# Performance work log

Measured on AMD Instinct MI355X. Metric: run time of the kernel, lower is better.

Reference implementation:

```python
import jax, jax.numpy as jnp
import numpy as np

N_NODES = 100000
N_EDGES = 1600000
IN_CH = 128
HID = 128
NUM_CLASSES = 10
NUM_GRAPHS = 128
SLOPE = 0.01  # F.leaky_relu default negative_slope


def _lin_params(key, fan_in, fan_out):
    kw, kb = jax.random.split(key)
    bound = 1.0 / np.sqrt(fan_in)
    W = jax.random.uniform(kw, (fan_in, fan_out), jnp.float32, -bound, bound)
    b = jax.random.uniform(kb, (fan_out,), jnp.float32, -bound, bound)
    return W, b


def setup_inputs() -> dict:
    key = jax.random.key(0)
    ks = jax.random.split(key, 8)
    x = jax.random.normal(ks[0], (N_NODES, IN_CH), jnp.float32)
    edge_index = jax.random.randint(ks[1], (2, N_EDGES), 0, N_NODES, jnp.int64)
    batch = jnp.sort(jax.random.randint(ks[2], (N_NODES,), 0, NUM_GRAPHS, jnp.int64))
    W1, b1 = _lin_params(ks[3], IN_CH, HID)
    W2, b2 = _lin_params(ks[4], HID, HID)
    W3, b3 = _lin_params(ks[5], HID, HID // 2)
    W4, b4 = _lin_params(ks[6], HID // 2, HID // 2)
    W5, b5 = _lin_params(ks[7], HID // 2, NUM_CLASSES)
    return {"x": x, "edge_index": edge_index, "batch": batch,
            "W1": W1, "b1": b1, "W2": W2, "b2": b2,
            "W3": W3, "b3": b3, "W4": W4, "b4": b4, "W5": W5, "b5": b5}


def gcn_conv(x, src, dst, W, b):
    # PyG GCNConv: h = x W; add self-loops; symmetric norm D^-1/2 (A+I) D^-1/2
    h = x @ W  # [N, F]
    n = x.shape[0]
    deg = jnp.zeros((n,), h.dtype).at[dst].add(1.0) + 1.0  # includes self-loop
    dinv = jax.lax.rsqrt(deg)
    norm = dinv[src] * dinv[dst]  # [E]
    agg = jnp.zeros_like(h).at[dst].add(h[src] * norm[:, None])
    agg = agg + h * (dinv * dinv)[:, None]  # self-loop term: 1/deg
    return agg + b


def reference(x, edge_index, batch, W1, b1, W2, b2, W3, b3, W4, b4, W5, b5):
    src, dst = edge_index[0], edge_index[1]
    h = jax.nn.leaky_relu(gcn_conv(x, src, dst, W1, b1), SLOPE)
    h = jax.nn.leaky_relu(gcn_conv(h, src, dst, W2, b2), SLOPE)
    # global mean pool over graphs
    sums = jax.ops.segment_sum(h, batch, num_segments=NUM_GRAPHS)
    cnts = jax.ops.segment_sum(jnp.ones((h.shape[0],), h.dtype), batch,
                               num_segments=NUM_GRAPHS)
    g = sums / jnp.maximum(cnts, 1.0)[:, None]  # [NUM_GRAPHS, HID]
    g = jax.nn.leaky_relu(g @ W3 + b3, SLOPE)
    g = jax.nn.leaky_relu(g @ W4 + b4, SLOPE)
    return g @ W5 + b5
```

## Files before the change

kernel.cpp:

```cpp
#include <hip/hip_runtime.h>
#include <hip/hip_bf16.h>


#define SLOPE 0.01f

__device__ __forceinline__ float lrelu(float x) { return x > 0.f ? x : SLOPE * x; }

__device__ __forceinline__ unsigned short f2bf(float f) {
    union { float f; unsigned u; } v; v.f = f;
    unsigned r = v.u + 0x7fffu + ((v.u >> 16) & 1u);
    return (unsigned short)(r >> 16);
}
__device__ __forceinline__ float bf2f(unsigned short h) {
    union { unsigned u; float f; } v; v.u = ((unsigned)h) << 16;
    return v.f;
}
__device__ __forceinline__ float bf_lo(unsigned x) {
    union { unsigned u; float f; } v; v.u = x << 16; return v.f;
}
__device__ __forceinline__ float bf_hi(unsigned x) {
    union { unsigned u; float f; } v; v.u = x & 0xffff0000u; return v.f;
}
__device__ __forceinline__ unsigned packbf(float lo, float hi) {
    return (unsigned)f2bf(lo) | ((unsigned)f2bf(hi) << 16);
}

typedef __attribute__((ext_vector_type(8))) short bf16x8;
typedef __attribute__((ext_vector_type(4))) float f32x4;
typedef __attribute__((ext_vector_type(2))) float f32x2;

#define LDA 136
#define CAPP 5120
#define MAXBUCK 400

__global__ void k_init(int* __restrict__ zbase, int nz,
                       const float* __restrict__ W1, unsigned short* __restrict__ WT1,
                       const float* __restrict__ W2, unsigned short* __restrict__ WT2) {
    int b = blockIdx.x;
    if (b < 64) {
        int idx = b * 256 + threadIdx.x;
        int k = idx >> 7, n = idx & 127;
        WT1[n * 128 + k] = f2bf(W1[idx]);
    } else if (b < 128) {
        int idx = (b - 64) * 256 + threadIdx.x;
        int k = idx >> 7, n = idx & 127;
        WT2[n * 128 + k] = f2bf(W2[idx]);
    } else {
        int i = (b - 128) * 256 + threadIdx.x;
        if (i < nz) zbase[i] = 0;
    }
}

template<bool IN_BF16, bool SCALE>
__device__ __forceinline__ void gemm_body(const void* __restrict__ Xv,
                                          const unsigned short* __restrict__ WT,
                                          unsigned short* __restrict__ Y, int M,
                                          unsigned short* Bs, int bid,
                                          const float* __restrict__ dinvg) {
    int t = threadIdx.x;
    int row0 = bid * 64;
    int w = t >> 6, l = t & 63;
    int lr = l & 15;
    int ko = (l >> 4) * 8;

    int gr = row0 + w * 16 + lr;
    bool inb = gr < M;
    bf16x8 afr[4];
    if (IN_BF16) {
        const unsigned short* Xrow = (const unsigned short*)Xv + (size_t)gr * 128;
#pragma unroll
        for (int kc = 0; kc < 4; ++kc) {
            if (inb) afr[kc] = *(const bf16x8*)&Xrow[kc * 32 + ko];
            else     afr[kc] = (bf16x8){0, 0, 0, 0, 0, 0, 0, 0};
        }
    } else {
        const float* Xrow = (const float*)Xv + (size_t)gr * 128;
#pragma unroll
        for (int kc = 0; kc < 4; ++kc) {
            if (inb) {
                float4 u0 = *(const float4*)&Xrow[kc * 32 + ko];
                float4 u1 = *(const float4*)&Xrow[kc * 32 + ko + 4];
                union { bf16x8 v; unsigned u[4]; } cv;
                cv.u[0] = packbf(u0.x, u0.y);
                cv.u[1] = packbf(u0.z, u0.w);
                cv.u[2] = packbf(u1.x, u1.y);
                cv.u[3] = packbf(u1.z, u1.w);
                afr[kc] = cv.v;
            } else afr[kc] = (bf16x8){0, 0, 0, 0, 0, 0, 0, 0};
        }
    }

    {
        const uint4* WT4 = (const uint4*)WT;
#pragma unroll
        for (int i = 0; i < 8; ++i) {
            int idx = t + i * 256;
            int n = idx >> 4, c8 = idx & 15;
            *(uint4*)&Bs[n * LDA + c8 * 8] = WT4[idx];
        }
    }
    __syncthreads();

    f32x4 acc[8];
#pragma unroll
    for (int c = 0; c < 8; ++c) acc[c] = (f32x4){0.f, 0.f, 0.f, 0.f};

#pragma unroll
    for (int kc = 0; kc < 4; ++kc) {
        int kb = kc * 32 + ko;
        bf16x8 bfr[8];
#pragma unroll
        for (int ct = 0; ct < 8; ++ct)
            bfr[ct] = *(const bf16x8*)&Bs[(ct * 16 + lr) * LDA + kb];
#pragma unroll
        for (int ct = 0; ct < 8; ++ct)
            acc[ct] = __builtin_amdgcn_mfma_f32_16x16x32_bf16(afr[kc], bfr[ct], acc[ct], 0, 0, 0);
    }

    __syncthreads();
    int qr = (l >> 4) * 4;
#pragma unroll
    for (int i = 0; i < 4; ++i) {
        int r = w * 16 + qr + i;
        float sc = 1.f;
        if (SCALE) {
            int gr2 = row0 + r;
            sc = (gr2 < M) ? dinvg[gr2] : 1.f;
        }
#pragma unroll
        for (int ct = 0; ct < 8; ++ct)
            Bs[r * LDA + ct * 16 + lr] = f2bf(acc[ct][i] * sc);
    }
    __syncthreads();
    {
        uint4* Y4 = (uint4*)Y;
#pragma unroll
        for (int i = 0; i < 4; ++i) {
            int idx = t + i * 256;
            int r = idx >> 4, c8 = idx & 15;
            int g2 = row0 + r;
            if (g2 < M) Y4[(size_t)g2 * 16 + c8] = *(const uint4*)&Bs[r * LDA + c8 * 8];
        }
    }
}

__device__ __forceinline__ void p1_body(const int* __restrict__ src,
                                        const int* __restrict__ dst,
                                        int E, int nb, int* __restrict__ g_cnt,
                                        unsigned* __restrict__ part,
                                        int* hist, int bid) {
    int* base = hist + MAXBUCK;
    int t = threadIdx.x;
    for (int b = t; b < nb; b += 256) hist[b] = 0;
    __syncthreads();
    int e0b = bid * 4096;
#pragma unroll
    for (int j = 0; j < 4; ++j) {
        int e = e0b + j * 1024 + t * 4;
        if (e + 3 < E) {
            int4 d = *(const int4*)&dst[e];
            atomicAdd(&hist[d.x >> 8], 1);
            atomicAdd(&hist[d.y >> 8], 1);
            atomicAdd(&hist[d.z >> 8], 1);
            atomicAdd(&hist[d.w >> 8], 1);
        } else {
            for (int k = e; k < E && k < e + 4; ++k)
                atomicAdd(&hist[dst[k] >> 8], 1);
        }
    }
    __syncthreads();
    for (int b = t; b < nb; b += 256) {
        int c = hist[b];
        base[b] = c ? atomicAdd(&g_cnt[b], c) : 0;
        hist[b] = 0;
    }
    __syncthreads();
#pragma unroll
    for (int j = 0; j < 4; ++j) {
        int e = e0b + j * 1024 + t * 4;
        if (e + 3 < E) {
            int4 d = *(const int4*)&dst[e];
            int4 s = *(const int4*)&src[e];
            int bk, p;
            bk = d.x >> 8; p = base[bk] + atomicAdd(&hist[bk], 1);
            if (p < CAPP) part[(size_t)bk * CAPP + p] = ((unsigned)s.x << 8) | ((unsigned)d.x & 255u);
            bk = d.y >> 8; p = base[bk] + atomicAdd(&hist[bk], 1);
            if (p < CAPP) part[(size_t)bk * CAPP + p] = ((unsigned)s.y << 8) | ((unsigned)d.y & 255u);
            bk = d.z >> 8; p = base[bk] + atomicAdd(&hist[bk], 1);
            if (p < CAPP) part[(size_t)bk * CAPP + p] = ((unsigned)s.z << 8) | ((unsigned)d.z & 255u);
            bk = d.w >> 8; p = base[bk] + atomicAdd(&hist[bk], 1);
            if (p < CAPP) part[(size_t)bk * CAPP + p] = ((unsigned)s.w << 8) | ((unsigned)d.w & 255u);
        } else {
            for (int k = e; k < E && k < e + 4; ++k) {
                int bk = dst[k] >> 8;
                int p = base[bk] + atomicAdd(&hist[bk], 1);
                if (p < CAPP) part[(size_t)bk * CAPP + p] = ((unsigned)src[k] << 8) | ((unsigned)dst[k] & 255u);
            }
        }
    }
}

__global__ __launch_bounds__(256) void k_p1_gemm1(
    const int* __restrict__ src, const int* __restrict__ dst, int E, int nb,
    int* __restrict__ g_cnt, unsigned* __restrict__ part, int nbP1,
    const float* __restrict__ X, const unsigned short* __restrict__ WT,
    unsigned short* __restrict__ Y, int M) {
    __shared__ __align__(16) unsigned short Bs[128 * LDA];
    int b = blockIdx.x;
    if (b < nbP1) p1_body(src, dst, E, nb, g_cnt, part, (int*)Bs, b);
    else gemm_body<false, false>((const void*)X, WT, Y, M, Bs, b - nbP1, nullptr);
}

__global__ __launch_bounds__(256) void k_p2(const unsigned* __restrict__ part,
                                            const int* __restrict__ g_cnt,
                                            int* __restrict__ csr,
                                            int2* __restrict__ rpz,
                                            float* __restrict__ dinvg,
                                            unsigned short* __restrict__ H, int N) {
    __shared__ int cnt[256];
    __shared__ int sc[256];
    __shared__ float dvl[256];
    int b = blockIdx.x, t = threadIdx.x;
    int nbase = b << 8;
    int nn = N - nbase; if (nn > 256) nn = 256;

    cnt[t] = 0;
    __syncthreads();

    int Eb = g_cnt[b]; if (Eb > CAPP) Eb = CAPP;
    const unsigned* pp = part + (size_t)b * CAPP;
    for (int i = t; i < Eb; i += 256)
        atomicAdd(&cnt[pp[i] & 255u], 1);
    __syncthreads();

    int v = cnt[t];
    sc[t] = v;
    __syncthreads();
    for (int off = 1; off < 256; off <<= 1) {
        int add = (t >= off) ? sc[t - off] : 0;
        __syncthreads();
        sc[t] += add;
        __syncthreads();
    }
    int excl = sc[t] - v;

    float di = rsqrtf((float)v + 1.0f);
    if (t < nn) {
        rpz[nbase + t] = make_int2(b * CAPP + excl, b * CAPP + excl + v);
        dinvg[nbase + t] = di;
    }
    dvl[t] = di;
    cnt[t] = excl;
    __syncthreads();

    for (int i = t; i < Eb; i += 256) {
        unsigned pv = pp[i];
        int lcl = pv & 255u;
        int p = atomicAdd(&cnt[lcl], 1);
        csr[(size_t)b * CAPP + p] = (int)(pv >> 8);
    }

    uint4* H4 = (uint4*)H;
    int tot = nn * 16;
    for (int i = t; i < tot; i += 256) {
        int r = i >> 4, c = i & 15;
        float d = dvl[r];
        uint4 hv = H4[(size_t)(nbase + r) * 16 + c];
        uint4 o;
        o.x = packbf(bf_lo(hv.x) * d, bf_hi(hv.x) * d);
        o.y = packbf(bf_lo(hv.y) * d, bf_hi(hv.y) * d);
        o.z = packbf(bf_lo(hv.z) * d, bf_hi(hv.z) * d);
        o.w = packbf(bf_lo(hv.w) * d, bf_hi(hv.w) * d);
        H4[(size_t)(nbase + r) * 16 + c] = o;
    }
}

__global__ __launch_bounds__(256) void k_gemm2(
    const void* __restrict__ Xv, const unsigned short* __restrict__ WT,
    unsigned short* __restrict__ Y, int M, const float* __restrict__ dinvg) {
    __shared__ __align__(16) unsigned short Bs[128 * LDA];
    gemm_body<true, true>(Xv, WT, Y, M, Bs, blockIdx.x, dinvg);
}

__device__ __forceinline__ void acc8(f32x2& S0, f32x2& S1, f32x2& S2, f32x2& S3,
                                     uint4 hv) {
    f32x2 t;
    t.x = bf_lo(hv.x); t.y = bf_hi(hv.x); S0 += t;
    t.x = bf_lo(hv.y); t.y = bf_hi(hv.y); S1 += t;
    t.x = bf_lo(hv.z); t.y = bf_hi(hv.z); S2 += t;
    t.x = bf_lo(hv.w); t.y = bf_hi(hv.w); S3 += t;
}

__global__ __launch_bounds__(256) void k_agg7(const unsigned short* __restrict__ H,
                                              const int* __restrict__ csr,
                                              const int2* __restrict__ rpz,
                                              const float* __restrict__ dinvg,
                                              const float* __restrict__ bias,
                                              unsigned short* __restrict__ OUT, int N) {
    int t = threadIdx.x;
    int grp = t >> 4, cl = t & 15;
    int u = blockIdx.x * 16 + grp;
    if (u >= N) return;
    const uint4* H4 = (const uint4*)H;

    int2 rz = rpz[u];
    int e0 = rz.x, e1 = rz.y;
    uint4 hs = H4[(size_t)u * 16 + cl];
    float du = dinvg[u];

    f32x2 A0 = {0.f, 0.f}, A1 = {0.f, 0.f}, A2 = {0.f, 0.f}, A3 = {0.f, 0.f};
    f32x2 B0 = {0.f, 0.f}, B1 = {0.f, 0.f}, B2 = {0.f, 0.f}, B3 = {0.f, 0.f};

    int e = e0;
    while (e < e1) {
        int nn = e1 - e; if (nn > 16) nn = 16;
        int ci = (cl < nn) ? csr[e + cl] : 0;
        int j = 0;
        for (; j + 4 <= nn; j += 4) {
            int i0 = __shfl(ci, j,     16);
            int i1 = __shfl(ci, j + 1, 16);
            int i2 = __shfl(ci, j + 2, 16);
            int i3 = __shfl(ci, j + 3, 16);
            uint4 hA = H4[(size_t)i0 * 16 + cl];
            uint4 hB = H4[(size_t)i1 * 16 + cl];
            uint4 hC = H4[(size_t)i2 * 16 + cl];
            uint4 hD = H4[(size_t)i3 * 16 + cl];
            acc8(A0, A1, A2, A3, hA);
            acc8(B0, B1, B2, B3, hB);
            acc8(A0, A1, A2, A3, hC);
            acc8(B0, B1, B2, B3, hD);
        }
        for (; j < nn; ++j) {
            int i0 = __shfl(ci, j, 16);
            uint4 hA = H4[(size_t)i0 * 16 + cl];
            acc8(A0, A1, A2, A3, hA);
        }
        e += nn;
    }

    acc8(A0, A1, A2, A3, hs);
    A0 += B0; A1 += B1; A2 += B2; A3 += B3;
    float a0 = A0.x, a1 = A0.y, a2 = A1.x, a3 = A1.y;
    float a4 = A2.x, a5 = A2.y, a6 = A3.x, a7 = A3.y;

    float4 c0 = *(const float4*)&bias[cl * 8];
    float4 c1 = *(const float4*)&bias[cl * 8 + 4];
    uint4 o;
    o.x = packbf(lrelu(a0 * du + c0.x), lrelu(a1 * du + c0.y));
    o.y = packbf(lrelu(a2 * du + c0.z), lrelu(a3 * du + c0.w));
    o.z = packbf(lrelu(a4 * du + c1.x), lrelu(a5 * du + c1.y));
    o.w = packbf(lrelu(a6 * du + c1.z), lrelu(a7 * du + c1.w));
    ((uint4*)OUT)[(size_t)u * 16 + cl] = o;
}

#define PCH 128
__global__ __launch_bounds__(256) void k_pool3(const unsigned short* __restrict__ H,
                                               const int* __restrict__ batch,
                                               float* __restrict__ Gsum,
                                               int* __restrict__ Gcnt, int N) {
    int t = threadIdx.x;
    int st = t >> 6, c2 = t & 63;
    int n0 = blockIdx.x * PCH + st * (PCH / 4);
    int n1 = n0 + (PCH / 4); if (n1 > N) n1 = N;
    if (n0 >= N) return;
    float a0 = 0.f, a1 = 0.f;
    int cur = batch[n0], runstart = n0;
    for (int n = n0; n < n1; ++n) {
        int g = batch[n];
        if (g != cur) {
            atomicAdd(&Gsum[cur * 128 + c2 * 2], a0);
            atomicAdd(&Gsum[cur * 128 + c2 * 2 + 1], a1);
            if (c2 == 0) atomicAdd(&Gcnt[cur], n - runstart);
            a0 = a1 = 0.f; cur = g; runstart = n;
        }
        unsigned hv = *(const unsigned*)&H[(size_t)n * 128 + c2 * 2];
        a0 += bf_lo(hv); a1 += bf_hi(hv);
    }
    atomicAdd(&Gsum[cur * 128 + c2 * 2], a0);
    atomicAdd(&Gsum[cur * 128 + c2 * 2 + 1], a1);
    if (c2 == 0) atomicAdd(&Gcnt[cur], n1 - runstart);
}

__global__ __launch_bounds__(64) void k_mlp(const float* __restrict__ Gsum,
                                            const int* __restrict__ Gcnt,
                                            const float* __restrict__ W3, const float* __restrict__ b3,
                                            const float* __restrict__ W4, const float* __restrict__ b4,
                                            const float* __restrict__ W5, const float* __restrict__ b5,
                                            float* __restrict__ OUT) {
    __shared__ float row[128];
    __shared__ float t1[64];
    __shared__ float t2[64];
    int g = blockIdx.x, t = threadIdx.x;
    float inv = 1.0f / fmaxf((float)Gcnt[g], 1.0f);
    row[t]      = Gsum[g * 128 + t] * inv;
    row[t + 64] = Gsum[g * 128 + t + 64] * inv;
    __syncthreads();
    float acc = b3[t];
    for (int k = 0; k < 128; ++k) acc += row[k] * W3[k * 64 + t];
    t1[t] = lrelu(acc);
    __syncthreads();
    acc = b4[t];
    for (int k = 0; k < 64; ++k) acc += t1[k] * W4[k * 64 + t];
    t2[t] = lrelu(acc);
    __syncthreads();
    if (t < 10) {
        acc = b5[t];
        for (int k = 0; k < 64; ++k) acc += t2[k] * W5[k * 10 + t];
        OUT[g * 10 + t] = acc;
    }
}


extern "C" void kernel_launch(void* const* d_in, const int* in_sizes, int n_in,
                              void* d_out, int out_size, void* d_ws, size_t ws_size,
                              hipStream_t stream) {
    const float* x    = (const float*)d_in[0];
    const int*   ei   = (const int*)d_in[1];
    const int*   batch= (const int*)d_in[2];
    const float* W1   = (const float*)d_in[3];
    const float* b1   = (const float*)d_in[4];
    const float* W2   = (const float*)d_in[5];
    const float* b2   = (const float*)d_in[6];
    const float* W3   = (const float*)d_in[7];
    const float* b3   = (const float*)d_in[8];
    const float* W4   = (const float*)d_in[9];
    const float* b4   = (const float*)d_in[10];
    const float* W5   = (const float*)d_in[11];
    const float* b5   = (const float*)d_in[12];
    float* out = (float*)d_out;

    const int N = in_sizes[2];
    const int E = in_sizes[1] / 2;
    const int NG = 128;

    const int* src = ei;
    const int* dst = ei + E;

    char* w = (char*)d_ws;
    unsigned short* bufA = (unsigned short*)w; w += (size_t)N * 128 * 2;
    unsigned short* bufB = (unsigned short*)w; w += (size_t)N * 128 * 2;
    int*   g_cnt = (int*)w;   w += 512 * 4;
    float* gsum  = (float*)w; w += (size_t)NG * 128 * 4;
    int*   gcnt  = (int*)w;   w += (size_t)NG * 4;
    float* dinv  = (float*)w; w += (size_t)N * 4;
    int2*  rpz   = (int2*)w;  w += (size_t)N * 8;
    unsigned* part = (unsigned*)w; w += (size_t)MAXBUCK * CAPP * 4;
    int*   csr   = (int*)w;   w += (size_t)MAXBUCK * CAPP * 4;
    unsigned short* WT1 = (unsigned short*)w; w += 128 * 128 * 2;
    unsigned short* WT2 = (unsigned short*)w; w += 128 * 128 * 2;
    (void)ws_size; (void)n_in; (void)out_size;

    int nbB  = (N + 255) >> 8;
    int nbP1 = (E + 4095) / 4096;
    int nbG  = (N + 63) / 64;
    int nZero = 512 + NG * 128 + NG;
    int nbZ  = (nZero + 255) / 256;

    k_init<<<128 + nbZ, 256, 0, stream>>>(g_cnt, nZero, W1, WT1, W2, WT2);
    k_p1_gemm1<<<nbP1 + nbG, 256, 0, stream>>>(src, dst, E, nbB, g_cnt, part,
                                               nbP1, x, WT1, bufA, N);
    k_p2<<<nbB, 256, 0, stream>>>(part, g_cnt, csr, rpz, dinv, bufA, N);

    int nbA = (N + 15) / 16;

    k_agg7<<<nbA, 256, 0, stream>>>(bufA, csr, rpz, dinv, b1, bufB, N);
    k_gemm2<<<nbG, 256, 0, stream>>>(bufB, WT2, bufA, N, dinv);
    k_agg7<<<nbA, 256, 0, stream>>>(bufA, csr, rpz, dinv, b2, bufB, N);

    int nbP = (N + PCH - 1) / PCH;
    k_pool3<<<nbP, 256, 0, stream>>>(bufB, batch, gsum, gcnt, N);
    k_mlp<<<NG, 64, 0, stream>>>(gsum, gcnt, W3, b3, W4, b4, W5, b5, out);
}
```

Measured before the change: 332.4 us.

## Fuse second aggregation with mean pooling and derive graph counts by binary search

Result: faster. 314.7 us (-5.3%).

```diff
diff --git a/kernel.cpp b/kernel.cpp
--- a/kernel.cpp
+++ b/kernel.cpp
@@ -11,10 +11,6 @@
     unsigned r = v.u + 0x7fffu + ((v.u >> 16) & 1u);
     return (unsigned short)(r >> 16);
 }
-__device__ __forceinline__ float bf2f(unsigned short h) {
-    union { unsigned u; float f; } v; v.u = ((unsigned)h) << 16;
-    return v.f;
-}
 __device__ __forceinline__ float bf_lo(unsigned x) {
     union { unsigned u; float f; } v; v.u = x << 16; return v.f;
 }
@@ -35,7 +31,9 @@
 
 __global__ void k_init(int* __restrict__ zbase, int nz,
                        const float* __restrict__ W1, unsigned short* __restrict__ WT1,
-                       const float* __restrict__ W2, unsigned short* __restrict__ WT2) {
+                       const float* __restrict__ W2, unsigned short* __restrict__ WT2,
+                       const int* __restrict__ batch, int* __restrict__ gstart,
+                       int N, int NG) {
     int b = blockIdx.x;
     if (b < 64) {
         int idx = b * 256 + threadIdx.x;
@@ -45,8 +43,15 @@
         int idx = (b - 64) * 256 + threadIdx.x;
         int k = idx >> 7, n = idx & 127;
         WT2[n * 128 + k] = f2bf(W2[idx]);
+    } else if (b == 128) {
+        int g = threadIdx.x;
+        if (g <= NG) {
+            int lo = 0, hi = N;
+            while (lo < hi) { int mid = (lo + hi) >> 1; if (batch[mid] < g) lo = mid + 1; else hi = mid; }
+            gstart[g] = lo;
+        }
     } else {
-        int i = (b - 128) * 256 + threadIdx.x;
+        int i = (b - 129) * 256 + threadIdx.x;
         if (i < nz) zbase[i] = 0;
     }
 }
@@ -291,23 +296,12 @@
     t.x = bf_lo(hv.w); t.y = bf_hi(hv.w); S3 += t;
 }
 
-__global__ __launch_bounds__(256) void k_agg7(const unsigned short* __restrict__ H,
-                                              const int* __restrict__ csr,
-                                              const int2* __restrict__ rpz,
-                                              const float* __restrict__ dinvg,
-                                              const float* __restrict__ bias,
-                                              unsigned short* __restrict__ OUT, int N) {
-    int t = threadIdx.x;
-    int grp = t >> 4, cl = t & 15;
-    int u = blockIdx.x * 16 + grp;
-    if (u >= N) return;
-    const uint4* H4 = (const uint4*)H;
-
-    int2 rz = rpz[u];
-    int e0 = rz.x, e1 = rz.y;
+__device__ __forceinline__ void agg_node_f(const uint4* __restrict__ H4,
+                                           const int* __restrict__ csr,
+                                           int e0, int e1, int u, float du,
+                                           const float* __restrict__ bias, int cl,
+                                           float* __restrict__ a) {
     uint4 hs = H4[(size_t)u * 16 + cl];
-    float du = dinvg[u];
-
     f32x2 A0 = {0.f, 0.f}, A1 = {0.f, 0.f}, A2 = {0.f, 0.f}, A3 = {0.f, 0.f};
     f32x2 B0 = {0.f, 0.f}, B1 = {0.f, 0.f}, B2 = {0.f, 0.f}, B3 = {0.f, 0.f};
 
@@ -340,49 +334,82 @@
 
     acc8(A0, A1, A2, A3, hs);
     A0 += B0; A1 += B1; A2 += B2; A3 += B3;
-    float a0 = A0.x, a1 = A0.y, a2 = A1.x, a3 = A1.y;
-    float a4 = A2.x, a5 = A2.y, a6 = A3.x, a7 = A3.y;
 
     float4 c0 = *(const float4*)&bias[cl * 8];
     float4 c1 = *(const float4*)&bias[cl * 8 + 4];
+    a[0] = lrelu(A0.x * du + c0.x); a[1] = lrelu(A0.y * du + c0.y);
+    a[2] = lrelu(A1.x * du + c0.z); a[3] = lrelu(A1.y * du + c0.w);
+    a[4] = lrelu(A2.x * du + c1.x); a[5] = lrelu(A2.y * du + c1.y);
+    a[6] = lrelu(A3.x * du + c1.z); a[7] = lrelu(A3.y * du + c1.w);
+}
+
+__global__ __launch_bounds__(256) void k_agg7(const unsigned short* __restrict__ H,
+                                              const int* __restrict__ csr,
+                                              const int2* __restrict__ rpz,
+                                              const float* __restrict__ dinvg,
+                                              const float* __restrict__ bias,
+                                              unsigned short* __restrict__ OUT, int N) {
+    int t = threadIdx.x;
+    int grp = t >> 4, cl = t & 15;
+    int u = blockIdx.x * 16 + grp;
+    if (u >= N) return;
+    const uint4* H4 = (const uint4*)H;
+    int2 rz = rpz[u];
+    float du = dinvg[u];
+    float a[8];
+    agg_node_f(H4, csr, rz.x, rz.y, u, du, bias, cl, a);
     uint4 o;
-    o.x = packbf(lrelu(a0 * du + c0.x), lrelu(a1 * du + c0.y));
-    o.y = packbf(lrelu(a2 * du + c0.z), lrelu(a3 * du + c0.w));
-    o.z = packbf(lrelu(a4 * du + c1.x), lrelu(a5 * du + c1.y));
-    o.w = packbf(lrelu(a6 * du + c1.z), lrelu(a7 * du + c1.w));
+    o.x = packbf(a[0], a[1]);
+    o.y = packbf(a[2], a[3]);
+    o.z = packbf(a[4], a[5]);
+    o.w = packbf(a[6], a[7]);
     ((uint4*)OUT)[(size_t)u * 16 + cl] = o;
 }
 
-#define PCH 128
-__global__ __launch_bounds__(256) void k_pool3(const unsigned short* __restrict__ H,
+__global__ __launch_bounds__(256) void k_agg7p(const unsigned short* __restrict__ H,
+                                               const int* __restrict__ csr,
+                                               const int2* __restrict__ rpz,
+                                               const float* __restrict__ dinvg,
+                                               const float* __restrict__ bias,
                                                const int* __restrict__ batch,
-                                               float* __restrict__ Gsum,
-                                               int* __restrict__ Gcnt, int N) {
+                                               float* __restrict__ Gsum, int N) {
+    __shared__ float P[16][132];
+    __shared__ int gb[16];
     int t = threadIdx.x;
-    int st = t >> 6, c2 = t & 63;
-    int n0 = blockIdx.x * PCH + st * (PCH / 4);
-    int n1 = n0 + (PCH / 4); if (n1 > N) n1 = N;
-    if (n0 >= N) return;
-    float a0 = 0.f, a1 = 0.f;
-    int cur = batch[n0], runstart = n0;
-    for (int n = n0; n < n1; ++n) {
-        int g = batch[n];
-        if (g != cur) {
-            atomicAdd(&Gsum[cur * 128 + c2 * 2], a0);
-            atomicAdd(&Gsum[cur * 128 + c2 * 2 + 1], a1);
-            if (c2 == 0) atomicAdd(&Gcnt[cur], n - runstart);
-            a0 = a1 = 0.f; cur = g; runstart = n;
-        }
-        unsigned hv = *(const unsigned*)&H[(size_t)n * 128 + c2 * 2];
-        a0 += bf_lo(hv); a1 += bf_hi(hv);
-    }
-    atomicAdd(&Gsum[cur * 128 + c2 * 2], a0);
-    atomicAdd(&Gsum[cur * 128 + c2 * 2 + 1], a1);
-    if (c2 == 0) atomicAdd(&Gcnt[cur], n1 - runstart);
+    int grp = t >> 4, cl = t & 15;
+    int u = blockIdx.x * 16 + grp;
+    if (blockIdx.x * 16 >= N) return;
+
+    float a[8] = {0.f, 0.f, 0.f, 0.f, 0.f, 0.f, 0.f, 0.f};
+    if (u < N) {
+        const uint4* H4 = (const uint4*)H;
+        int2 rz = rpz[u];
+        float du = dinvg[u];
+        agg_node_f(H4, csr, rz.x, rz.y, u, du, bias, cl, a);
+    }
+    if (cl == 0) gb[grp] = (u < N) ? batch[u] : -1;
+#pragma unroll
+    for (int j = 0; j < 8; ++j) P[grp][cl * 8 + j] = a[j];
+    __syncthreads();
+
+    if (t < 128) {
+        float run = 0.f;
+        int cur = -1;
+        for (int i = 0; i < 16; ++i) {
+            int g = gb[i];
+            if (g < 0) break;
+            if (g != cur) {
+                if (cur >= 0) atomicAdd(&Gsum[cur * 128 + t], run);
+                run = 0.f; cur = g;
+            }
+            run += P[i][t];
+        }
+        if (cur >= 0) atomicAdd(&Gsum[cur * 128 + t], run);
+    }
 }
 
 __global__ __launch_bounds__(64) void k_mlp(const float* __restrict__ Gsum,
-                                            const int* __restrict__ Gcnt,
+                                            const int* __restrict__ gstart,
                                             const float* __restrict__ W3, const float* __restrict__ b3,
                                             const float* __restrict__ W4, const float* __restrict__ b4,
                                             const float* __restrict__ W5, const float* __restrict__ b5,
@@ -391,7 +418,7 @@
     __shared__ float t1[64];
     __shared__ float t2[64];
     int g = blockIdx.x, t = threadIdx.x;
-    float inv = 1.0f / fmaxf((float)Gcnt[g], 1.0f);
+    float inv = 1.0f / fmaxf((float)(gstart[g + 1] - gstart[g]), 1.0f);
     row[t]      = Gsum[g * 128 + t] * inv;
     row[t + 64] = Gsum[g * 128 + t + 64] * inv;
     __syncthreads();
@@ -441,7 +468,7 @@
     unsigned short* bufB = (unsigned short*)w; w += (size_t)N * 128 * 2;
     int*   g_cnt = (int*)w;   w += 512 * 4;
     float* gsum  = (float*)w; w += (size_t)NG * 128 * 4;
-    int*   gcnt  = (int*)w;   w += (size_t)NG * 4;
+    int*   gstart= (int*)w;   w += 512 * 4;
     float* dinv  = (float*)w; w += (size_t)N * 4;
     int2*  rpz   = (int2*)w;  w += (size_t)N * 8;
     unsigned* part = (unsigned*)w; w += (size_t)MAXBUCK * CAPP * 4;
@@ -453,10 +480,11 @@
     int nbB  = (N + 255) >> 8;
     int nbP1 = (E + 4095) / 4096;
     int nbG  = (N + 63) / 64;
-    int nZero = 512 + NG * 128 + NG;
+    int nZero = 512 + NG * 128;
     int nbZ  = (nZero + 255) / 256;
 
-    k_init<<<128 + nbZ, 256, 0, stream>>>(g_cnt, nZero, W1, WT1, W2, WT2);
+    k_init<<<129 + nbZ, 256, 0, stream>>>(g_cnt, nZero, W1, WT1, W2, WT2,
+                                          batch, gstart, N, NG);
     k_p1_gemm1<<<nbP1 + nbG, 256, 0, stream>>>(src, dst, E, nbB, g_cnt, part,
                                                nbP1, x, WT1, bufA, N);
     k_p2<<<nbB, 256, 0, stream>>>(part, g_cnt, csr, rpz, dinv, bufA, N);
@@ -465,9 +493,7 @@
 
     k_agg7<<<nbA, 256, 0, stream>>>(bufA, csr, rpz, dinv, b1, bufB, N);
     k_gemm2<<<nbG, 256, 0, stream>>>(bufB, WT2, bufA, N, dinv);
-    k_agg7<<<nbA, 256, 0, stream>>>(bufA, csr, rpz, dinv, b2, bufB, N);
-
-    int nbP = (N + PCH - 1) / PCH;
-    k_pool3<<<nbP, 256, 0, stream>>>(bufB, batch, gsum, gcnt, N);
-    k_mlp<<<NG, 64, 0, stream>>>(gsum, gcnt, W3, b3, W4, b4, W5, b5, out);
-}
+    k_agg7p<<<nbA, 256, 0, stream>>>(bufA, csr, rpz, dinv, b2, batch, gsum, N);
+
+    k_mlp<<<NG, 64, 0, stream>>>(gsum, gstart, W3, b3, W4, b4, W5, b5, out);
+}
```
